# Optimization experiments

Measured on AMD Instinct MI355X. Metric: run time of the kernel, lower is better.

Reference implementation:

```python
import jax, jax.numpy as jnp
import numpy as np

B, T, C, H = 16, 512, 1080, 20  # batch, seq, embd, heads; head_dim = C // H = 54

def setup_inputs() -> dict:
    key = jax.random.key(0)
    k1, k2, k3, k4, k5 = jax.random.split(key, 5)
    s = 0.02
    return {
        "x": jax.random.normal(k1, (B, T, C), dtype=jnp.float32),
        "W_attn": jax.random.normal(k2, (C, 3 * C), dtype=jnp.float32) * s,
        "b_attn": jax.random.normal(k3, (3 * C,), dtype=jnp.float32) * s,
        "W_proj": jax.random.normal(k4, (C, C), dtype=jnp.float32) * s,
        "b_proj": jax.random.normal(k5, (C,), dtype=jnp.float32) * s,
    }

def reference(x, W_attn, b_attn, W_proj, b_proj):
    Bb, Tt, Cc = x.shape
    hd = Cc // H
    qkv = jnp.einsum('btc,cd->btd', x, W_attn) + b_attn  # [B,T,3C]
    q, k, v = jnp.split(qkv, 3, axis=2)
    # [B,T,C] -> [B,H,T,hd]
    q = q.reshape(Bb, Tt, H, hd).transpose(0, 2, 1, 3)
    k = k.reshape(Bb, Tt, H, hd).transpose(0, 2, 1, 3)
    v = v.reshape(Bb, Tt, H, hd).transpose(0, 2, 1, 3)
    att = jnp.einsum('bhqd,bhkd->bhqk', q, k) * (1.0 / jnp.sqrt(jnp.float32(hd)))
    causal = jnp.tril(jnp.ones((Tt, Tt), dtype=bool))
    att = jnp.where(causal, att, -jnp.inf)
    att = jax.nn.softmax(att, axis=-1)
    y = jnp.einsum('bhqk,bhkd->bhqd', att, v)  # [B,H,T,hd]
    y = y.transpose(0, 2, 1, 3).reshape(Bb, Tt, Cc)
    return jnp.einsum('btc,cd->btd', y, W_proj) + b_proj
```

## Files before the change

kernel.cpp:

```cpp
#include <hip/hip_runtime.h>
#include <hip/hip_bf16.h>

#define B_   16
#define T_   512
#define C_   1080
#define H_   20
#define HD_  54
#define DP_  64
#define M_   (B_ * T_)
#define KP_  1088
#define NT_  17
#define NQKV_ 3840
#define NPRJ_ 1152
#define NBT_ (B_ * H_ * T_)

typedef short bf16x8 __attribute__((ext_vector_type(8)));
typedef float f32x4  __attribute__((ext_vector_type(4)));
typedef unsigned short u16x8 __attribute__((ext_vector_type(8)));

__device__ __forceinline__ void gload_lds16(const void* g, void* l) {
    __builtin_amdgcn_global_load_lds(
        (const __attribute__((address_space(1))) void*)g,
        (__attribute__((address_space(3))) void*)l,
        16, 0, 0);
}

__device__ __forceinline__ unsigned short f2b(float x) {
    return __builtin_bit_cast(unsigned short, __float2bfloat16(x));
}

#define PB_CVT  8704
#define PB_WTA  4080
#define PB_WTP  1224
__global__ __launch_bounds__(256) void prep_all(
    const float* __restrict__ x, const float* __restrict__ W_attn,
    const float* __restrict__ W_proj, const float* __restrict__ b_attn,
    __hip_bfloat16* __restrict__ xb,
    __hip_bfloat16* __restrict__ wta, __hip_bfloat16* __restrict__ wtp,
    float* __restrict__ bp)
{
    __shared__ float tile[32][33];
    int id = blockIdx.x;

    if (id < PB_CVT) {
        int idx = id * 256 + threadIdx.x;
        int m = idx / (KP_ / 4), c = idx - m * (KP_ / 4);
        ushort4 o;
        if (c < C_ / 4) {
            float4 v = *reinterpret_cast<const float4*>(x + (size_t)m * C_ + c * 4);
            o.x = f2b(v.x); o.y = f2b(v.y); o.z = f2b(v.z); o.w = f2b(v.w);
        } else {
            o.x = o.y = o.z = o.w = 0;
        }
        *reinterpret_cast<ushort4*>(reinterpret_cast<unsigned short*>(xb) +
                                    (size_t)m * KP_ + c * 4) = o;
        return;
    }
    id -= PB_CVT;
    const int tx = threadIdx.x & 31, ty = threadIdx.x >> 5;

    if (id < PB_WTA) {
        int bx = id % 120, by = id / 120;
        int n0 = bx * 32, k0 = by * 32;
        int np = n0 + tx;
        int which = np / 1280;
        int rem = np - which * 1280;
        int h = rem >> 6, d = rem & 63;
        int sn = which * C_ + h * HD_ + d;
        bool valid = d < HD_;
        #pragma unroll
        for (int i = 0; i < 32; i += 8) {
            int k = k0 + ty + i;
            tile[ty + i][tx] = (valid && k < C_) ? W_attn[(size_t)k * (3 * C_) + sn] : 0.f;
        }
        __syncthreads();
        #pragma unroll
        for (int i = 0; i < 32; i += 8) {
            int n = n0 + ty + i, k = k0 + tx;
            wta[(size_t)n * KP_ + k] = __float2bfloat16(tile[tx][ty + i]);
        }
        return;
    }
    id -= PB_WTA;

    if (id < PB_WTP) {
        int bx = id % 36, by = id / 36;
        int n0 = bx * 32, k0 = by * 32;
        #pragma unroll
        for (int i = 0; i < 32; i += 8) {
            int k = k0 + ty + i, n = n0 + tx;
            tile[ty + i][tx] = (k < C_ && n < C_) ? W_proj[(size_t)k * C_ + n] : 0.f;
        }
        __syncthreads();
        #pragma unroll
        for (int i = 0; i < 32; i += 8) {
            int n = n0 + ty + i, k = k0 + tx;
            wtp[(size_t)n * KP_ + k] = __float2bfloat16(tile[tx][ty + i]);
        }
        return;
    }
    id -= PB_WTP;

    {
        int i = id * 256 + threadIdx.x;
        if (i < NQKV_) {
            int which = i / 1280, rem = i - which * 1280;
            int h = rem >> 6, d = rem & 63;
            float v = (d < HD_) ? b_attn[which * C_ + h * HD_ + d] : 0.f;
            if (which == 2 && d == 63) v = 1.0f;
            bp[i] = v;
        }
    }
}

__global__ __launch_bounds__(512, 2) void gemm256(
    const unsigned short* __restrict__ A,
    const unsigned short* __restrict__ Bt,
    const float* __restrict__ bias,
    unsigned short* __restrict__ outQ,
    unsigned short* __restrict__ outK,
    unsigned short* __restrict__ outV)
{
    __shared__ __align__(16) char smem[131072];

    const int tid  = threadIdx.x;
    const int lane = tid & 63;
    const int wv   = tid >> 6;
    const int wr   = wv >> 2;
    const int wc   = wv & 3;
    const int lq   = lane & 15;
    const int lg   = lane >> 4;

    const int id  = blockIdx.y * 15 + blockIdx.x;
    const int xcd = id & 7;
    const int j   = id >> 3;
    const int m0  = (xcd * 4 + (j & 3)) * 256;
    const int n0  = (j >> 2) * 256;

    unsigned gA[2], gB[2];
    const int ld0 = tid * 16, ld1 = tid * 16 + 8192;
    #pragma unroll
    for (int i = 0; i < 2; ++i) {
        int ci = tid + i * 512;
        int r  = ci >> 3;
        int kc = (ci & 7) ^ (r & 7);
        gA[i] = (unsigned)(m0 + r) * KP_ + kc * 8;
        gB[i] = (unsigned)(n0 + r) * KP_ + kc * 8;
    }
    const unsigned HALFSTEP = 128u * KP_;

    auto stage = [&](int buf, int hIdx, unsigned k0) {
        char* sb = smem + buf * 65536 +
                   (hIdx < 2 ? hIdx * 16384 : 32768 + (hIdx - 2) * 16384);
        const unsigned short* sp = (hIdx < 2) ? A : Bt;
        unsigned extra = (hIdx & 1) ? HALFSTEP : 0u;
        gload_lds16(sp + ((hIdx < 2) ? gA[0] : gB[0]) + extra + k0, sb + ld0);
        gload_lds16(sp + ((hIdx < 2) ? gA[1] : gB[1]) + extra + k0, sb + ld1);
    };

    const int s0 = (lg ^ (lq & 7)) * 16;
    const int s1 = ((4 + lg) ^ (lq & 7)) * 16;
    const int aBase = wr * 16384 + lq * 128;
    const int bBase = 32768 + (wc >> 1) * 16384 + (wc & 1) * 8192 + lq * 128;

    f32x4 acc[8][4] = {};

    stage(0, 0, 0); stage(0, 1, 0); stage(0, 2, 0); stage(0, 3, 0);

    for (int t = 0; t < NT_; ++t) {
        const int cur = t & 1;
        if (t + 1 < NT_) {
            const int nb = cur ^ 1;
            const unsigned k0n = (unsigned)(t + 1) * 64;
            stage(nb, 0, k0n); stage(nb, 1, k0n); stage(nb, 2, k0n); stage(nb, 3, k0n);
            asm volatile("s_waitcnt vmcnt(8)" ::: "memory");
        } else {
            asm volatile("s_waitcnt vmcnt(0)" ::: "memory");
        }
        __builtin_amdgcn_s_barrier();

        const char* Ab = smem + cur * 65536 + aBase;
        const char* Bb = smem + cur * 65536 + bBase;

        bf16x8 bfr[4][2];
        #pragma unroll
        for (int ni = 0; ni < 4; ++ni) {
            bfr[ni][0] = *reinterpret_cast<const bf16x8*>(Bb + ni * 2048 + s0);
            bfr[ni][1] = *reinterpret_cast<const bf16x8*>(Bb + ni * 2048 + s1);
        }
        bf16x8 afA[2][2], afB[2][2];
        #pragma unroll
        for (int i = 0; i < 2; ++i) {
            afA[0][i] = *reinterpret_cast<const bf16x8*>(Ab + i * 2048 + s0);
            afA[1][i] = *reinterpret_cast<const bf16x8*>(Ab + i * 2048 + s1);
        }
        __builtin_amdgcn_s_setprio(1);
        #pragma unroll
        for (int q = 0; q < 4; ++q) {
            if (q < 3) {
                #pragma unroll
                for (int i = 0; i < 2; ++i) {
                    if (q & 1) {
                        afA[0][i] = *reinterpret_cast<const bf16x8*>(Ab + ((q + 1) * 2 + i) * 2048 + s0);
                        afA[1][i] = *reinterpret_cast<const bf16x8*>(Ab + ((q + 1) * 2 + i) * 2048 + s1);
                    } else {
                        afB[0][i] = *reinterpret_cast<const bf16x8*>(Ab + ((q + 1) * 2 + i) * 2048 + s0);
                        afB[1][i] = *reinterpret_cast<const bf16x8*>(Ab + ((q + 1) * 2 + i) * 2048 + s1);
                    }
                }
            }
            #pragma unroll
            for (int kk = 0; kk < 2; ++kk)
                #pragma unroll
                for (int i = 0; i < 2; ++i)
                    #pragma unroll
                    for (int ni = 0; ni < 4; ++ni)
                        acc[q * 2 + i][ni] = __builtin_amdgcn_mfma_f32_16x16x32_bf16(
                            (q & 1) ? afB[kk][i] : afA[kk][i], bfr[ni][kk],
                            acc[q * 2 + i][ni], 0, 0, 0);
        }
        __builtin_amdgcn_s_setprio(0);
        __builtin_amdgcn_s_barrier();
    }

    const int which = n0 / 1280;
    if (which < 2) {
        unsigned short* dst = which ? outK : outQ;
        #pragma unroll
        for (int mi = 0; mi < 8; ++mi) {
            int mg = m0 + wr * 128 + mi * 16 + lg * 4;
            int b = mg >> 9, t0 = mg & (T_ - 1);
            #pragma unroll
            for (int ni = 0; ni < 4; ++ni) {
                int nl = wc * 64 + ni * 16 + lq;
                int ng = n0 + nl - which * 1280;
                int h = ng >> 6, d = ng & 63;
                float bs = bias[n0 + nl];
                size_t basei = ((size_t)(b * H_ + h) * T_ + t0) * DP_ + d;
                #pragma unroll
                for (int j2 = 0; j2 < 4; ++j2)
                    dst[basei + (size_t)j2 * DP_] = f2b(acc[mi][ni][j2] + bs);
            }
        }
    } else {
        unsigned short* lt = (unsigned short*)smem;
        #pragma unroll
        for (int hm = 0; hm < 2; ++hm) {
            if (hm == 1) __syncthreads();
            if (wr == hm) {
                #pragma unroll
                for (int mi = 0; mi < 8; ++mi) {
                    int ml = mi * 16 + lg * 4;
                    int mc = ml >> 3, mo = ml & 7;
                    #pragma unroll
                    for (int ni = 0; ni < 4; ++ni) {
                        int nl = wc * 64 + ni * 16 + lq;
                        float bs = bias[n0 + nl];
                        ushort4 pk;
                        pk.x = f2b(acc[mi][ni][0] + bs);
                        pk.y = f2b(acc[mi][ni][1] + bs);
                        pk.z = f2b(acc[mi][ni][2] + bs);
                        pk.w = f2b(acc[mi][ni][3] + bs);
                        int slot = mc ^ ((nl >> 3) & 15);
                        *reinterpret_cast<ushort4*>(lt + nl * 136 + slot * 8 + mo) = pk;
                    }
                }
            }
            __syncthreads();
            #pragma unroll
            for (int it = 0; it < 8; ++it) {
                int idx = it * 512 + tid;
                int c2 = idx >> 4, j2 = idx & 15;
                int slot = j2 ^ ((c2 >> 3) & 15);
                u16x8 v = *reinterpret_cast<const u16x8*>(lt + c2 * 136 + slot * 8);
                int ng = n0 + c2 - 2560;
                int h = ng >> 6, d = ng & 63;
                int mg = m0 + hm * 128 + j2 * 8;
                int b = mg >> 9, t = mg & (T_ - 1);
                *reinterpret_cast<u16x8*>(outV + ((size_t)(b * H_ + h) * DP_ + d) * T_ + t) = v;
            }
        }
    }
}

__global__ __launch_bounds__(256) void gemm_mfma_p(
    const unsigned short* __restrict__ A,
    const unsigned short* __restrict__ Bt,
    const float* __restrict__ bias,
    float* __restrict__ outP)
{
    __shared__ __align__(16) char smem[65536];

    const int tid  = threadIdx.x;
    const int lane = tid & 63;
    const int wv   = tid >> 6;
    const int wm   = (wv >> 1) * 64;
    const int wn   = (wv & 1) * 64;
    const int lr   = lane & 15;
    const int lk   = lane >> 4;

    const int gx  = gridDim.x;
    const int gy  = gridDim.y;
    const int id  = blockIdx.y * gx + blockIdx.x;
    const int xcd = id & 7;
    const int j   = id >> 3;
    const int mpc = gy >> 3;
    const int m0  = (xcd * mpc + j % mpc) * 128;
    const int n0  = (j / mpc) * 128;

    unsigned aOff[4], bOff[4];
    int ciB[4];
    #pragma unroll
    for (int it = 0; it < 4; ++it) {
        int ci = it * 256 + tid;
        int r = ci >> 3, p = ci & 7;
        int kc = p ^ (r & 7);
        aOff[it] = (unsigned)(m0 + r) * KP_ + kc * 8;
        bOff[it] = (unsigned)(n0 + r) * KP_ + kc * 8;
        ciB[it] = ci * 16;
    }
    int aRd[2][4], bRd[2][4];
    #pragma unroll
    for (int kk = 0; kk < 2; ++kk) {
        #pragma unroll
        for (int mi = 0; mi < 4; ++mi) {
            int row = wm + mi * 16 + lr;
            aRd[kk][mi] = row * 128 + ((kk * 4 + lk) ^ (row & 7)) * 16;
            int rowb = wn + mi * 16 + lr;
            bRd[kk][mi] = 16384 + rowb * 128 + ((kk * 4 + lk) ^ (rowb & 7)) * 16;
        }
    }

    f32x4 acc[4][4] = {};

    auto stage = [&](int buf, int kt) {
        const unsigned k0 = kt * 64;
        char* sb = smem + buf * 32768;
        #pragma unroll
        for (int it = 0; it < 4; ++it)
            gload_lds16(A + aOff[it] + k0, sb + ciB[it]);
        #pragma unroll
        for (int it = 0; it < 4; ++it)
            gload_lds16(Bt + bOff[it] + k0, sb + 16384 + ciB[it]);
    };

    stage(0, 0);
    for (int kt = 0; kt < NT_; ++kt) {
        const int c = kt & 1;
        if (kt + 1 < NT_) {
            stage(1 - c, kt + 1);
            asm volatile("s_waitcnt vmcnt(8)" ::: "memory");
        } else {
            asm volatile("s_waitcnt vmcnt(0)" ::: "memory");
        }
        __builtin_amdgcn_s_barrier();
        asm volatile("" ::: "memory");

        const char* base = smem + c * 32768;
        #pragma unroll
        for (int kk = 0; kk < 2; ++kk) {
            bf16x8 af[4], bfr[4];
            #pragma unroll
            for (int mi = 0; mi < 4; ++mi)
                af[mi] = *reinterpret_cast<const bf16x8*>(base + aRd[kk][mi]);
            #pragma unroll
            for (int ni = 0; ni < 4; ++ni)
                bfr[ni] = *reinterpret_cast<const bf16x8*>(base + bRd[kk][ni]);
            #pragma unroll
            for (int mi = 0; mi < 4; ++mi)
                #pragma unroll
                for (int ni = 0; ni < 4; ++ni)
                    acc[mi][ni] = __builtin_amdgcn_mfma_f32_16x16x32_bf16(
                        af[mi], bfr[ni], acc[mi][ni], 0, 0, 0);
        }
        asm volatile("" ::: "memory");
        __builtin_amdgcn_s_barrier();
    }

    #pragma unroll
    for (int mi = 0; mi < 4; ++mi) {
        int mrow = m0 + wm + mi * 16 + lk * 4;
        #pragma unroll
        for (int ni = 0; ni < 4; ++ni) {
            int n = n0 + wn + ni * 16 + lr;
            if (n < C_) {
                float bs = bias[n];
                #pragma unroll
                for (int j2 = 0; j2 < 4; ++j2)
                    outP[(size_t)(mrow + j2) * C_ + n] = acc[mi][ni][j2] + bs;
            }
        }
    }
}

__global__ __launch_bounds__(512) void attn_mfma(
    const unsigned short* __restrict__ Q, const unsigned short* __restrict__ K,
    const unsigned short* __restrict__ Vt, __hip_bfloat16* __restrict__ Y)
{
    __shared__ __align__(16) char kvs[16384];
    __shared__ __align__(16) unsigned short ps[8][16][72];

    const int tid  = threadIdx.x;
    const int lane = tid & 63;
    const int wv   = tid >> 6;
    const int grp  = wv >> 2;
    const int wq   = wv & 3;
    const int lq   = lane & 15;
    const int lg   = lane >> 4;
    const int bh   = blockIdx.y;
    const int qt_own = blockIdx.x * 2 + grp;
    const int qbase  = qt_own * 64;
    const float cs = 0.13608276348795434f * 1.44269504f;

    bf16x8 qf[2];
    {
        const unsigned short* qp = Q + ((size_t)bh * T_ + qbase + wq * 16 + lq) * DP_;
        qf[0] = *reinterpret_cast<const bf16x8*>(qp + lg * 8);
        qf[1] = *reinterpret_cast<const bf16x8*>(qp + 32 + lg * 8);
    }

    const int sr = tid >> 3, sp = tid & 7;
    const int spc = sp ^ (sr & 7);
    const unsigned kOff = (unsigned)(sr * DP_ + spc * 8);
    const unsigned vOff = (unsigned)(sr * T_ + spc * 8);
    const unsigned short* Kb = K  + (size_t)bh * T_ * DP_;
    const unsigned short* Vb = Vt + (size_t)bh * DP_ * T_;

    f32x4 o[4] = {};
    unsigned short* pbase = &ps[wv][0][0];
    const int nt = blockIdx.x * 2 + 2;

    for (int kt = 0; kt < nt; ++kt) {
        const int kbase = kt * 64;
        gload_lds16(Kb + kOff + (unsigned)kbase * DP_, kvs + tid * 16);
        gload_lds16(Vb + vOff + (unsigned)kbase, kvs + 8192 + tid * 16);
        __syncthreads();

        if (kt <= qt_own) {
            f32x4 s[4] = {};
            __builtin_amdgcn_s_setprio(1);
            #pragma unroll
            for (int dc = 0; dc < 2; ++dc) {
                #pragma unroll
                for (int ni = 0; ni < 4; ++ni) {
                    int row = ni * 16 + lq;
                    int ch  = (dc * 4 + lg) ^ (row & 7);
                    bf16x8 kf = *reinterpret_cast<const bf16x8*>(kvs + row * 128 + ch * 16);
                    s[ni] = __builtin_amdgcn_mfma_f32_16x16x32_bf16(qf[dc], kf, s[ni], 0, 0, 0);
                }
            }
            __builtin_amdgcn_s_setprio(0);

            if (kt == qt_own) {
                #pragma unroll
                for (int ni = 0; ni < 4; ++ni) {
                    int kg = kbase + ni * 16 + lq;
                    #pragma unroll
                    for (int j = 0; j < 4; ++j) {
                        int qg = qbase + wq * 16 + lg * 4 + j;
                        s[ni][j] = (kg > qg) ? -3.0e38f : s[ni][j];
                    }
                }
            }
            #pragma unroll
            for (int ni = 0; ni < 4; ++ni) {
                #pragma unroll
                for (int j = 0; j < 4; ++j) {
                    float p = exp2f(s[ni][j] * cs);
                    int qr = lg * 4 + j;
                    int cidx = (ni * 2 + (lq >> 3)) ^ (qr & 7);
                    pbase[qr * 72 + cidx * 8 + (lq & 7)] = f2b(p);
                }
            }

            asm volatile("s_waitcnt lgkmcnt(0)" ::: "memory");
            __builtin_amdgcn_sched_barrier(0);

            __builtin_amdgcn_s_setprio(1);
            #pragma unroll
            for (int dc = 0; dc < 2; ++dc) {
                int cc = (dc * 4 + lg) ^ (lq & 7);
                bf16x8 pf = *reinterpret_cast<const bf16x8*>(pbase + lq * 72 + cc * 8);
                #pragma unroll
                for (int ni = 0; ni < 4; ++ni) {
                    int row = ni * 16 + lq;
                    int ch  = (dc * 4 + lg) ^ (row & 7);
                    bf16x8 vf = *reinterpret_cast<const bf16x8*>(kvs + 8192 + row * 128 + ch * 16);
                    o[ni] = __builtin_amdgcn_mfma_f32_16x16x32_bf16(pf, vf, o[ni], 0, 0, 0);
                }
            }
            __builtin_amdgcn_s_setprio(0);
        }
        __syncthreads();
    }

    const int b = bh / H_, h = bh - b * H_;
    #pragma unroll
    for (int j = 0; j < 4; ++j) {
        float l = __shfl(o[3][j], (lane & 48) | 15, 64);
        float inv = 1.f / l;
        int t = qbase + wq * 16 + lg * 4 + j;
        #pragma unroll
        for (int ni = 0; ni < 4; ++ni) {
            int d = ni * 16 + lq;
            if (d < HD_)
                Y[((size_t)b * T_ + t) * KP_ + h * HD_ + d] =
                    __float2bfloat16(o[ni][j] * inv);
        }
    }
}

extern "C" void kernel_launch(void* const* d_in, const int* in_sizes, int n_in,
                              void* d_out, int out_size, void* d_ws, size_t ws_size,
                              hipStream_t stream)
{
    const float* x      = (const float*)d_in[0];
    const float* W_attn = (const float*)d_in[1];
    const float* b_attn = (const float*)d_in[2];
    const float* W_proj = (const float*)d_in[3];
    const float* b_proj = (const float*)d_in[4];
    float* out = (float*)d_out;

    __hip_bfloat16* xb = (__hip_bfloat16*)d_ws;
    unsigned short* qb = (unsigned short*)(xb + (size_t)M_ * KP_);
    unsigned short* kb = qb + (size_t)NBT_ * DP_;
    unsigned short* vtb = kb + (size_t)NBT_ * DP_;
    __hip_bfloat16* wta = (__hip_bfloat16*)(vtb + (size_t)NBT_ * DP_);
    __hip_bfloat16* wtp = wta + (size_t)NQKV_ * KP_;
    float* bp = (float*)(wtp + (size_t)NPRJ_ * KP_);
    __hip_bfloat16* yb = xb;

    prep_all<<<PB_CVT + PB_WTA + PB_WTP + 15, 256, 0, stream>>>(
        x, W_attn, W_proj, b_attn, xb, wta, wtp, bp);

    gemm256<<<dim3(NQKV_ / 256, M_ / 256), 512, 0, stream>>>(
        (const unsigned short*)xb, (const unsigned short*)wta, bp,
        qb, kb, vtb);

    attn_mfma<<<dim3(T_ / 128, B_ * H_), 512, 0, stream>>>(qb, kb, vtb, yb);

    gemm_mfma_p<<<dim3(NPRJ_ / 128, M_ / 128), 256, 0, stream>>>(
        (const unsigned short*)yb, (const unsigned short*)wtp, b_proj, out);
}
```

Baseline: 169.2 us.

## Restructure QKV GEMM main loop with explicit LDS waitcnt pipelining and barrier placement

Reworks the K-loop of the QKV projection GEMM. The first tile is now waited for before the loop, the global-to-LDS wait for the next tile moves to the end of each iteration, and the A fragments are double-buffered with explicit lgkmcnt waits and sched_barriers. This lets LDS reads overlap MFMA groups and keeps the prefetch in flight during compute. It adds a mid-iteration barrier after the fragment loads, so the new buffer can be overwritten safely. The risk is extra barrier stalls, and scheduling constraints that limit what the compiler can reorder.

```diff
diff --git a/kernel.cpp b/kernel.cpp
--- a/kernel.cpp
+++ b/kernel.cpp
@@ -166,60 +166,101 @@
     f32x4 acc[8][4] = {};
 
     stage(0, 0, 0); stage(0, 1, 0); stage(0, 2, 0); stage(0, 3, 0);
+    asm volatile("s_waitcnt vmcnt(0)" ::: "memory");
+    __builtin_amdgcn_s_barrier();
 
     for (int t = 0; t < NT_; ++t) {
         const int cur = t & 1;
-        if (t + 1 < NT_) {
+        const bool pf = (t + 1 < NT_);
+        if (pf) {
             const int nb = cur ^ 1;
             const unsigned k0n = (unsigned)(t + 1) * 64;
             stage(nb, 0, k0n); stage(nb, 1, k0n); stage(nb, 2, k0n); stage(nb, 3, k0n);
-            asm volatile("s_waitcnt vmcnt(8)" ::: "memory");
-        } else {
-            asm volatile("s_waitcnt vmcnt(0)" ::: "memory");
-        }
-        __builtin_amdgcn_s_barrier();
-
+        }
         const char* Ab = smem + cur * 65536 + aBase;
         const char* Bb = smem + cur * 65536 + bBase;
 
-        bf16x8 bfr[4][2];
+        bf16x8 bfr[4][2], afX[2][2], afY[2][2];
         #pragma unroll
         for (int ni = 0; ni < 4; ++ni) {
             bfr[ni][0] = *reinterpret_cast<const bf16x8*>(Bb + ni * 2048 + s0);
             bfr[ni][1] = *reinterpret_cast<const bf16x8*>(Bb + ni * 2048 + s1);
         }
-        bf16x8 afA[2][2], afB[2][2];
         #pragma unroll
         for (int i = 0; i < 2; ++i) {
-            afA[0][i] = *reinterpret_cast<const bf16x8*>(Ab + i * 2048 + s0);
-            afA[1][i] = *reinterpret_cast<const bf16x8*>(Ab + i * 2048 + s1);
-        }
+            afX[0][i] = *reinterpret_cast<const bf16x8*>(Ab + (0 + i) * 2048 + s0);
+            afX[1][i] = *reinterpret_cast<const bf16x8*>(Ab + (0 + i) * 2048 + s1);
+        }
+        #pragma unroll
+        for (int i = 0; i < 2; ++i) {
+            afY[0][i] = *reinterpret_cast<const bf16x8*>(Ab + (2 + i) * 2048 + s0);
+            afY[1][i] = *reinterpret_cast<const bf16x8*>(Ab + (2 + i) * 2048 + s1);
+        }
+        __builtin_amdgcn_s_barrier();
+
+        asm volatile("s_waitcnt lgkmcnt(4)" ::: "memory");
+        __builtin_amdgcn_sched_barrier(0);
         __builtin_amdgcn_s_setprio(1);
         #pragma unroll
-        for (int q = 0; q < 4; ++q) {
-            if (q < 3) {
-                #pragma unroll
-                for (int i = 0; i < 2; ++i) {
-                    if (q & 1) {
-                        afA[0][i] = *reinterpret_cast<const bf16x8*>(Ab + ((q + 1) * 2 + i) * 2048 + s0);
-                        afA[1][i] = *reinterpret_cast<const bf16x8*>(Ab + ((q + 1) * 2 + i) * 2048 + s1);
-                    } else {
-                        afB[0][i] = *reinterpret_cast<const bf16x8*>(Ab + ((q + 1) * 2 + i) * 2048 + s0);
-                        afB[1][i] = *reinterpret_cast<const bf16x8*>(Ab + ((q + 1) * 2 + i) * 2048 + s1);
-                    }
-                }
-            }
-            #pragma unroll
-            for (int kk = 0; kk < 2; ++kk)
-                #pragma unroll
-                for (int i = 0; i < 2; ++i)
-                    #pragma unroll
-                    for (int ni = 0; ni < 4; ++ni)
-                        acc[q * 2 + i][ni] = __builtin_amdgcn_mfma_f32_16x16x32_bf16(
-                            (q & 1) ? afB[kk][i] : afA[kk][i], bfr[ni][kk],
-                            acc[q * 2 + i][ni], 0, 0, 0);
-        }
+        for (int kk = 0; kk < 2; ++kk)
+            #pragma unroll
+            for (int i = 0; i < 2; ++i)
+                #pragma unroll
+                for (int ni = 0; ni < 4; ++ni)
+                    acc[0 + i][ni] = __builtin_amdgcn_mfma_f32_16x16x32_bf16(
+                        afX[kk][i], bfr[ni][kk], acc[0 + i][ni], 0, 0, 0);
         __builtin_amdgcn_s_setprio(0);
+
+        #pragma unroll
+        for (int i = 0; i < 2; ++i) {
+            afX[0][i] = *reinterpret_cast<const bf16x8*>(Ab + (4 + i) * 2048 + s0);
+            afX[1][i] = *reinterpret_cast<const bf16x8*>(Ab + (4 + i) * 2048 + s1);
+        }
+        asm volatile("s_waitcnt lgkmcnt(4)" ::: "memory");
+        __builtin_amdgcn_sched_barrier(0);
+        __builtin_amdgcn_s_setprio(1);
+        #pragma unroll
+        for (int kk = 0; kk < 2; ++kk)
+            #pragma unroll
+            for (int i = 0; i < 2; ++i)
+                #pragma unroll
+                for (int ni = 0; ni < 4; ++ni)
+                    acc[2 + i][ni] = __builtin_amdgcn_mfma_f32_16x16x32_bf16(
+                        afY[kk][i], bfr[ni][kk], acc[2 + i][ni], 0, 0, 0);
+        __builtin_amdgcn_s_setprio(0);
+
+        #pragma unroll
+        for (int i = 0; i < 2; ++i) {
+            afY[0][i] = *reinterpret_cast<const bf16x8*>(Ab + (6 + i) * 2048 + s0);
+            afY[1][i] = *reinterpret_cast<const bf16x8*>(Ab + (6 + i) * 2048 + s1);
+        }
+        asm volatile("s_waitcnt lgkmcnt(4)" ::: "memory");
+        __builtin_amdgcn_sched_barrier(0);
+        __builtin_amdgcn_s_setprio(1);
+        #pragma unroll
+        for (int kk = 0; kk < 2; ++kk)
+            #pragma unroll
+            for (int i = 0; i < 2; ++i)
+                #pragma unroll
+                for (int ni = 0; ni < 4; ++ni)
+                    acc[4 + i][ni] = __builtin_amdgcn_mfma_f32_16x16x32_bf16(
+                        afX[kk][i], bfr[ni][kk], acc[4 + i][ni], 0, 0, 0);
+        __builtin_amdgcn_s_setprio(0);
+
+        asm volatile("s_waitcnt lgkmcnt(0)" ::: "memory");
+        __builtin_amdgcn_sched_barrier(0);
+        __builtin_amdgcn_s_setprio(1);
+        #pragma unroll
+        for (int kk = 0; kk < 2; ++kk)
+            #pragma unroll
+            for (int i = 0; i < 2; ++i)
+                #pragma unroll
+                for (int ni = 0; ni < 4; ++ni)
+                    acc[6 + i][ni] = __builtin_amdgcn_mfma_f32_16x16x32_bf16(
+                        afY[kk][i], bfr[ni][kk], acc[6 + i][ni], 0, 0, 0);
+        __builtin_amdgcn_s_setprio(0);
+
+        if (pf) asm volatile("s_waitcnt vmcnt(0)" ::: "memory");
         __builtin_amdgcn_s_barrier();
     }
 
```

Measured after the change: 166.9 us. About the same (-1.4%).

## Restructure GEMM main loop into fine-grained interleaved load/MFMA schedule

Applied to the files above, without the earlier changes.

Rewrites the QKV/proj GEMM K-loop as an unrolled two-tile-per-iteration schedule. Global-to-LDS staging of individual half-tiles is interleaved between four MFMA quads, separated by barriers and explicit lgkmcnt waits, instead of issuing all loads for the next tile at once. The aim is to spread memory traffic across the compute phase and keep MFMA units busy. It adds many more workgroup barriers per K-step, which may cost more in synchronisation than the overlap gains.

```diff
diff --git a/kernel.cpp b/kernel.cpp
--- a/kernel.cpp
+++ b/kernel.cpp
@@ -113,6 +113,17 @@
     }
 }
 
+#define BAR_() __builtin_amdgcn_s_barrier()
+#define LGKM0_() do { asm volatile("s_waitcnt lgkmcnt(0)" ::: "memory"); \
+                      __builtin_amdgcn_sched_barrier(0); } while (0)
+#define MFMA_QUAD(Q) do { __builtin_amdgcn_s_setprio(1);                      \
+    _Pragma("unroll") for (int kk = 0; kk < 2; ++kk)                          \
+    _Pragma("unroll") for (int i = 0; i < 2; ++i)                             \
+    _Pragma("unroll") for (int ni = 0; ni < 4; ++ni)                          \
+        acc[(Q) * 2 + i][ni] = __builtin_amdgcn_mfma_f32_16x16x32_bf16(       \
+            af[kk][i], bfr[ni][kk], acc[(Q) * 2 + i][ni], 0, 0, 0);           \
+    __builtin_amdgcn_s_setprio(0); } while (0)
+
 __global__ __launch_bounds__(512, 2) void gemm256(
     const unsigned short* __restrict__ A,
     const unsigned short* __restrict__ Bt,
@@ -163,65 +174,77 @@
     const int aBase = wr * 16384 + lq * 128;
     const int bBase = 32768 + (wc >> 1) * 16384 + (wc & 1) * 8192 + lq * 128;
 
-    f32x4 acc[8][4] = {};
-
-    stage(0, 0, 0); stage(0, 1, 0); stage(0, 2, 0); stage(0, 3, 0);
-
-    for (int t = 0; t < NT_; ++t) {
-        const int cur = t & 1;
-        if (t + 1 < NT_) {
-            const int nb = cur ^ 1;
-            const unsigned k0n = (unsigned)(t + 1) * 64;
-            stage(nb, 0, k0n); stage(nb, 1, k0n); stage(nb, 2, k0n); stage(nb, 3, k0n);
-            asm volatile("s_waitcnt vmcnt(8)" ::: "memory");
-        } else {
-            asm volatile("s_waitcnt vmcnt(0)" ::: "memory");
-        }
-        __builtin_amdgcn_s_barrier();
-
-        const char* Ab = smem + cur * 65536 + aBase;
-        const char* Bb = smem + cur * 65536 + bBase;
-
-        bf16x8 bfr[4][2];
+    auto readA = [&](const char* Ab, int q, bf16x8 (&af)[2][2]) {
+        #pragma unroll
+        for (int i = 0; i < 2; ++i) {
+            af[0][i] = *reinterpret_cast<const bf16x8*>(Ab + (q * 2 + i) * 2048 + s0);
+            af[1][i] = *reinterpret_cast<const bf16x8*>(Ab + (q * 2 + i) * 2048 + s1);
+        }
+    };
+    auto readB = [&](const char* Bb, bf16x8 (&bfr)[4][2]) {
         #pragma unroll
         for (int ni = 0; ni < 4; ++ni) {
             bfr[ni][0] = *reinterpret_cast<const bf16x8*>(Bb + ni * 2048 + s0);
             bfr[ni][1] = *reinterpret_cast<const bf16x8*>(Bb + ni * 2048 + s1);
         }
-        bf16x8 afA[2][2], afB[2][2];
-        #pragma unroll
-        for (int i = 0; i < 2; ++i) {
-            afA[0][i] = *reinterpret_cast<const bf16x8*>(Ab + i * 2048 + s0);
-            afA[1][i] = *reinterpret_cast<const bf16x8*>(Ab + i * 2048 + s1);
-        }
-        __builtin_amdgcn_s_setprio(1);
-        #pragma unroll
-        for (int q = 0; q < 4; ++q) {
-            if (q < 3) {
-                #pragma unroll
-                for (int i = 0; i < 2; ++i) {
-                    if (q & 1) {
-                        afA[0][i] = *reinterpret_cast<const bf16x8*>(Ab + ((q + 1) * 2 + i) * 2048 + s0);
-                        afA[1][i] = *reinterpret_cast<const bf16x8*>(Ab + ((q + 1) * 2 + i) * 2048 + s1);
-                    } else {
-                        afB[0][i] = *reinterpret_cast<const bf16x8*>(Ab + ((q + 1) * 2 + i) * 2048 + s0);
-                        afB[1][i] = *reinterpret_cast<const bf16x8*>(Ab + ((q + 1) * 2 + i) * 2048 + s1);
-                    }
-                }
-            }
-            #pragma unroll
-            for (int kk = 0; kk < 2; ++kk)
-                #pragma unroll
-                for (int i = 0; i < 2; ++i)
-                    #pragma unroll
-                    for (int ni = 0; ni < 4; ++ni)
-                        acc[q * 2 + i][ni] = __builtin_amdgcn_mfma_f32_16x16x32_bf16(
-                            (q & 1) ? afB[kk][i] : afA[kk][i], bfr[ni][kk],
-                            acc[q * 2 + i][ni], 0, 0, 0);
-        }
-        __builtin_amdgcn_s_setprio(0);
-        __builtin_amdgcn_s_barrier();
-    }
+    };
+
+    f32x4 acc[8][4] = {};
+
+    stage(0, 2, 0); stage(0, 3, 0);
+    stage(0, 0, 0); stage(0, 1, 0);
+    stage(1, 2, 64); stage(1, 3, 64);
+    asm volatile("s_waitcnt vmcnt(4)" ::: "memory");
+    BAR_();
+
+    const char* Ab0 = smem + aBase;
+    const char* Bb0 = smem + bBase;
+    const char* Ab1 = smem + 65536 + aBase;
+    const char* Bb1 = smem + 65536 + bBase;
+
+    for (int it = 0; it < 8; ++it) {
+        const unsigned kT1 = (unsigned)(2 * it + 1) * 64;
+        const unsigned kT2 = (unsigned)(2 * it + 2) * 64;
+        const unsigned kT3 = (unsigned)(2 * it + 3) * 64;
+        const bool lastIt = (it == 7);
+        bf16x8 bfr[4][2], af[2][2];
+
+        readB(Bb0, bfr); readA(Ab0, 0, af);
+        stage(1, 0, kT1); stage(1, 1, kT1);
+        BAR_(); LGKM0_(); MFMA_QUAD(0); BAR_();
+        readA(Ab0, 1, af);
+        stage(0, 2, kT2);
+        BAR_(); LGKM0_(); MFMA_QUAD(1); BAR_();
+        readA(Ab0, 2, af);
+        stage(0, 3, kT2);
+        BAR_(); LGKM0_(); MFMA_QUAD(2); BAR_();
+        readA(Ab0, 3, af);
+        asm volatile("s_waitcnt vmcnt(4)" ::: "memory");
+        BAR_(); LGKM0_(); MFMA_QUAD(3); BAR_();
+        readB(Bb1, bfr); readA(Ab1, 0, af);
+        stage(0, 0, kT2); stage(0, 1, kT2);
+        BAR_(); LGKM0_(); MFMA_QUAD(0); BAR_();
+        readA(Ab1, 1, af);
+        if (!lastIt) stage(1, 2, kT3);
+        BAR_(); LGKM0_(); MFMA_QUAD(1); BAR_();
+        readA(Ab1, 2, af);
+        if (!lastIt) stage(1, 3, kT3);
+        BAR_(); LGKM0_(); MFMA_QUAD(2); BAR_();
+        readA(Ab1, 3, af);
+        if (!lastIt) asm volatile("s_waitcnt vmcnt(4)" ::: "memory");
+        else         asm volatile("s_waitcnt vmcnt(0)" ::: "memory");
+        BAR_(); LGKM0_(); MFMA_QUAD(3); BAR_();
+    }
+
+    {
+        bf16x8 bfr[4][2], af[2][2];
+        readB(Bb0, bfr);
+        readA(Ab0, 0, af); LGKM0_(); MFMA_QUAD(0);
+        readA(Ab0, 1, af); LGKM0_(); MFMA_QUAD(1);
+        readA(Ab0, 2, af); LGKM0_(); MFMA_QUAD(2);
+        readA(Ab0, 3, af); LGKM0_(); MFMA_QUAD(3);
+    }
+    __syncthreads();
 
     const int which = n0 / 1280;
     if (which < 2) {
```

After: 163.0 us (median of 2 runs). 3.7% less time.

## Shrink QKV GEMM K-tile to 32 to cut LDS footprint

Applied to the files above, without the earlier changes.

The QKV projection GEMM now stages K-slices of 32 instead of 64, which halves the double-buffered LDS footprint from 128KB to about 68KB. The LDS swizzle and fragment addressing are rewritten to a 4-chunk XOR pattern, and the software prefetch of A fragments inside the MFMA loop is simplified. The intent is to relieve LDS pressure so two 512-thread blocks can be resident per CU, as the launch bounds request. In exchange it doubles the number of barrier-separated iterations and gives each iteration less MFMA work to hide load latency.

```diff
diff --git a/kernel.cpp b/kernel.cpp
--- a/kernel.cpp
+++ b/kernel.cpp
@@ -10,6 +10,7 @@
 #define M_   (B_ * T_)
 #define KP_  1088
 #define NT_  17
+#define NT32_ 34
 #define NQKV_ 3840
 #define NPRJ_ 1152
 #define NBT_ (B_ * H_ * T_)
@@ -121,7 +122,7 @@
     unsigned short* __restrict__ outK,
     unsigned short* __restrict__ outV)
 {
-    __shared__ __align__(16) char smem[131072];
+    __shared__ __align__(16) char smem[69632];
 
     const int tid  = threadIdx.x;
     const int lane = tid & 63;
@@ -137,88 +138,62 @@
     const int m0  = (xcd * 4 + (j & 3)) * 256;
     const int n0  = (j >> 2) * 256;
 
-    unsigned gA[2], gB[2];
-    const int ld0 = tid * 16, ld1 = tid * 16 + 8192;
+    unsigned aOff[2], bOff[2];
+    int dA[2];
     #pragma unroll
     for (int i = 0; i < 2; ++i) {
         int ci = tid + i * 512;
-        int r  = ci >> 3;
-        int kc = (ci & 7) ^ (r & 7);
-        gA[i] = (unsigned)(m0 + r) * KP_ + kc * 8;
-        gB[i] = (unsigned)(n0 + r) * KP_ + kc * 8;
-    }
-    const unsigned HALFSTEP = 128u * KP_;
-
-    auto stage = [&](int buf, int hIdx, unsigned k0) {
-        char* sb = smem + buf * 65536 +
-                   (hIdx < 2 ? hIdx * 16384 : 32768 + (hIdx - 2) * 16384);
-        const unsigned short* sp = (hIdx < 2) ? A : Bt;
-        unsigned extra = (hIdx & 1) ? HALFSTEP : 0u;
-        gload_lds16(sp + ((hIdx < 2) ? gA[0] : gB[0]) + extra + k0, sb + ld0);
-        gload_lds16(sp + ((hIdx < 2) ? gA[1] : gB[1]) + extra + k0, sb + ld1);
+        int r  = ci >> 2, c = ci & 3;
+        int kc = c ^ (r & 3);
+        aOff[i] = (unsigned)(m0 + r) * KP_ + kc * 8;
+        bOff[i] = (unsigned)(n0 + r) * KP_ + kc * 8;
+        dA[i] = ci * 16;
+    }
+
+    auto stage = [&](int buf, unsigned k0) {
+        char* sb = smem + buf * 32768;
+        gload_lds16(A + aOff[0] + k0, sb + dA[0]);
+        gload_lds16(A + aOff[1] + k0, sb + dA[1]);
+        gload_lds16(Bt + bOff[0] + k0, sb + 16384 + dA[0]);
+        gload_lds16(Bt + bOff[1] + k0, sb + 16384 + dA[1]);
     };
 
-    const int s0 = (lg ^ (lq & 7)) * 16;
-    const int s1 = ((4 + lg) ^ (lq & 7)) * 16;
-    const int aBase = wr * 16384 + lq * 128;
-    const int bBase = 32768 + (wc >> 1) * 16384 + (wc & 1) * 8192 + lq * 128;
+    const int s0 = (lg ^ (lq & 3)) * 16;
+    const int aBase = wr * 8192 + lq * 64 + s0;
+    const int bBase = 16384 + wc * 4096 + lq * 64 + s0;
 
     f32x4 acc[8][4] = {};
 
-    stage(0, 0, 0); stage(0, 1, 0); stage(0, 2, 0); stage(0, 3, 0);
-
-    for (int t = 0; t < NT_; ++t) {
+    stage(0, 0);
+    for (int t = 0; t < NT32_; ++t) {
         const int cur = t & 1;
-        if (t + 1 < NT_) {
-            const int nb = cur ^ 1;
-            const unsigned k0n = (unsigned)(t + 1) * 64;
-            stage(nb, 0, k0n); stage(nb, 1, k0n); stage(nb, 2, k0n); stage(nb, 3, k0n);
-            asm volatile("s_waitcnt vmcnt(8)" ::: "memory");
+        if (t + 1 < NT32_) {
+            stage(cur ^ 1, (unsigned)(t + 1) * 32);
+            asm volatile("s_waitcnt vmcnt(4)" ::: "memory");
         } else {
             asm volatile("s_waitcnt vmcnt(0)" ::: "memory");
         }
         __builtin_amdgcn_s_barrier();
 
-        const char* Ab = smem + cur * 65536 + aBase;
-        const char* Bb = smem + cur * 65536 + bBase;
-
-        bf16x8 bfr[4][2];
-        #pragma unroll
-        for (int ni = 0; ni < 4; ++ni) {
-            bfr[ni][0] = *reinterpret_cast<const bf16x8*>(Bb + ni * 2048 + s0);
-            bfr[ni][1] = *reinterpret_cast<const bf16x8*>(Bb + ni * 2048 + s1);
-        }
-        bf16x8 afA[2][2], afB[2][2];
-        #pragma unroll
-        for (int i = 0; i < 2; ++i) {
-            afA[0][i] = *reinterpret_cast<const bf16x8*>(Ab + i * 2048 + s0);
-            afA[1][i] = *reinterpret_cast<const bf16x8*>(Ab + i * 2048 + s1);
-        }
+        const char* Ab = smem + cur * 32768 + aBase;
+        const char* Bb = smem + cur * 32768 + bBase;
+
+        bf16x8 bfr[4];
+        #pragma unroll
+        for (int ni = 0; ni < 4; ++ni)
+            bfr[ni] = *reinterpret_cast<const bf16x8*>(Bb + ni * 1024);
+        bf16x8 af[8];
+        #pragma unroll
+        for (int mi = 0; mi < 8; ++mi)
+            af[mi] = *reinterpret_cast<const bf16x8*>(Ab + mi * 1024);
+
         __builtin_amdgcn_s_setprio(1);
         #pragma unroll
-        for (int q = 0; q < 4; ++q) {
-            if (q < 3) {
-                #pragma unroll
-                for (int i = 0; i < 2; ++i) {
-                    if (q & 1) {
-                        afA[0][i] = *reinterpret_cast<const bf16x8*>(Ab + ((q + 1) * 2 + i) * 2048 + s0);
-                        afA[1][i] = *reinterpret_cast<const bf16x8*>(Ab + ((q + 1) * 2 + i) * 2048 + s1);
-                    } else {
-                        afB[0][i] = *reinterpret_cast<const bf16x8*>(Ab + ((q + 1) * 2 + i) * 2048 + s0);
-                        afB[1][i] = *reinterpret_cast<const bf16x8*>(Ab + ((q + 1) * 2 + i) * 2048 + s1);
-                    }
-                }
-            }
-            #pragma unroll
-            for (int kk = 0; kk < 2; ++kk)
-                #pragma unroll
-                for (int i = 0; i < 2; ++i)
-                    #pragma unroll
-                    for (int ni = 0; ni < 4; ++ni)
-                        acc[q * 2 + i][ni] = __builtin_amdgcn_mfma_f32_16x16x32_bf16(
-                            (q & 1) ? afB[kk][i] : afA[kk][i], bfr[ni][kk],
-                            acc[q * 2 + i][ni], 0, 0, 0);
-        }
+        for (int mi = 0; mi < 8; ++mi)
+            #pragma unroll
+            for (int ni = 0; ni < 4; ++ni)
+                acc[mi][ni] = __builtin_amdgcn_mfma_f32_16x16x32_bf16(
+                    af[mi], bfr[ni], acc[mi][ni], 0, 0, 0);
         __builtin_amdgcn_s_setprio(0);
         __builtin_amdgcn_s_barrier();
     }
```

New measurement: 172.7 us. +2.1%, slower.
